# Kernel optimization log

Hardware: AMD Instinct MI355X
Metric: run time of the kernel (lower is better)

Reference implementation:

```python
import jax, jax.numpy as jnp
import numpy as np

N = 100000
E = 800000

def elu(x):
    return jnp.where(x > 0, x, jnp.expm1(x))

def transformer_conv(x, src, dst, ea, Wq, bq, Wk, bk, Wv, bv, We, Ws, bs, heads, ch):
    # PyG TransformerConv (concat=True, root_weight=True, beta=False, eval so dropout off)
    n = x.shape[0]
    q = (x @ Wq + bq).reshape(n, heads, ch)
    k = (x @ Wk + bk).reshape(n, heads, ch)
    v = (x @ Wv + bv).reshape(n, heads, ch)
    e = (ea @ We).reshape(-1, heads, ch)            # [E,H,C], lin_edge has no bias
    kj = k[src] + e                                  # [E,H,C]
    logits = (q[dst] * kj).sum(-1) / jnp.sqrt(jnp.float32(ch))  # [E,H]
    # segment softmax over incoming edges of each dst node
    m = jax.ops.segment_max(logits, dst, num_segments=n)
    ex = jnp.exp(logits - m[dst])
    denom = jax.ops.segment_sum(ex, dst, num_segments=n)
    alpha = ex / denom[dst]                          # [E,H]
    msg = alpha[..., None] * (v[src] + e)            # [E,H,C]
    agg = jax.ops.segment_sum(msg, dst, num_segments=n).reshape(n, heads * ch)
    return agg + x @ Ws + bs                         # skip connection (lin_skip)

def setup_inputs() -> dict:
    key = jax.random.key(0)
    ks = jax.random.split(key, 32)
    def rn(k, shape, scale=0.1):
        return jax.random.normal(k, shape, dtype=jnp.float32) * scale
    d = {}
    d['x'] = jax.random.normal(ks[0], (N, 23), dtype=jnp.float32)
    d['edge_index'] = jax.random.randint(ks[1], (2, E), 0, N, dtype=jnp.int32)
    d['edge_attr'] = jax.random.normal(ks[2], (E, 7), dtype=jnp.float32)
    d['linA_w'] = rn(ks[3], (23, 23)); d['linA_b'] = jnp.zeros((23,), jnp.float32)
    d['linB_w'] = rn(ks[4], (23, 23)); d['linB_b'] = jnp.zeros((23,), jnp.float32)
    # conv1: in=23, heads=8, out=24 -> 192
    d['q1_w'] = rn(ks[5], (23, 192)); d['q1_b'] = jnp.zeros((192,), jnp.float32)
    d['k1_w'] = rn(ks[6], (23, 192)); d['k1_b'] = jnp.zeros((192,), jnp.float32)
    d['v1_w'] = rn(ks[7], (23, 192)); d['v1_b'] = jnp.zeros((192,), jnp.float32)
    d['e1_w'] = rn(ks[8], (7, 192))
    d['s1_w'] = rn(ks[9], (23, 192)); d['s1_b'] = jnp.zeros((192,), jnp.float32)
    # conv4: in=192, heads=8, out=8 -> 64
    d['q2_w'] = rn(ks[10], (192, 64)); d['q2_b'] = jnp.zeros((64,), jnp.float32)
    d['k2_w'] = rn(ks[11], (192, 64)); d['k2_b'] = jnp.zeros((64,), jnp.float32)
    d['v2_w'] = rn(ks[12], (192, 64)); d['v2_b'] = jnp.zeros((64,), jnp.float32)
    d['e2_w'] = rn(ks[13], (7, 64))
    d['s2_w'] = rn(ks[14], (192, 64)); d['s2_b'] = jnp.zeros((64,), jnp.float32)
    d['lin1_w'] = rn(ks[15], (64, 20)); d['lin1_b'] = jnp.zeros((20,), jnp.float32)
    d['lin2_w'] = rn(ks[16], (20, 1)); d['lin2_b'] = jnp.zeros((1,), jnp.float32)
    return d

def reference(x, edge_index, edge_attr,
              linA_w, linA_b, linB_w, linB_b,
              q1_w, q1_b, k1_w, k1_b, v1_w, v1_b, e1_w, s1_w, s1_b,
              q2_w, q2_b, k2_w, k2_b, v2_w, v2_b, e2_w, s2_w, s2_b,
              lin1_w, lin1_b, lin2_w, lin2_b):
    src, dst = edge_index[0], edge_index[1]
    h = elu(x @ linA_w + linA_b)
    h = elu(h @ linB_w + linB_b)
    h = transformer_conv(h, src, dst, edge_attr, q1_w, q1_b, k1_w, k1_b, v1_w, v1_b, e1_w, s1_w, s1_b, 8, 24)
    h = elu(h)
    h = transformer_conv(h, src, dst, edge_attr, q2_w, q2_b, k2_w, k2_b, v2_w, v2_b, e2_w, s2_w, s2_b, 8, 8)
    h = elu(h)
    h = elu(h @ lin1_w + lin1_b)
    return h @ lin2_w + lin2_b
```

## Files before the change

kernel.cpp:

```cpp
#include <hip/hip_runtime.h>
#include <math.h>


__device__ __forceinline__ float elu_f(float x) {
    return x > 0.f ? x : expm1f(x);
}


__global__ void mlp_kernel(const float* __restrict__ x,
                           const float* __restrict__ A, const float* __restrict__ ab,
                           const float* __restrict__ B, const float* __restrict__ bb,
                           float* __restrict__ out, int n) {
    __shared__ float sA[23 * 23], sB[23 * 23], sa[23], sb[23];
    for (int t = threadIdx.x; t < 23 * 23; t += blockDim.x) { sA[t] = A[t]; sB[t] = B[t]; }
    if (threadIdx.x < 23) { sa[threadIdx.x] = ab[threadIdx.x]; sb[threadIdx.x] = bb[threadIdx.x]; }
    __syncthreads();
    int i = blockIdx.x * blockDim.x + threadIdx.x;
    if (i >= n) return;
    float xi[23], h1[23];
    #pragma unroll
    for (int j = 0; j < 23; j++) xi[j] = x[(size_t)i * 23 + j];
    #pragma unroll
    for (int o = 0; o < 23; o++) {
        float acc = sa[o];
        #pragma unroll
        for (int j = 0; j < 23; j++) acc = fmaf(xi[j], sA[j * 23 + o], acc);
        h1[o] = elu_f(acc);
    }
    #pragma unroll
    for (int o = 0; o < 23; o++) {
        float acc = sb[o];
        #pragma unroll
        for (int j = 0; j < 23; j++) acc = fmaf(h1[j], sB[j * 23 + o], acc);
        out[(size_t)i * 23 + o] = elu_f(acc);
    }
}

template<int IN, int Kc, int OUTW, int M, int TY, int KM, int VM>
__global__ void proj_tiled_kernel(const float* __restrict__ in, int n,
    const float* __restrict__ W0, const float* __restrict__ b0,
    const float* __restrict__ W1, const float* __restrict__ b1,
    const float* __restrict__ W2, const float* __restrict__ b2,
    const float* __restrict__ W3, const float* __restrict__ b3,
    float* __restrict__ kvout,
    float* __restrict__ r0, float* __restrict__ r1,
    float* __restrict__ r2, float* __restrict__ r3) {
    constexpr int WTOT = M * OUTW;
    constexpr int CG   = WTOT / 8;
    constexpr int BN   = TY * 4;
    constexpr int SAW  = BN + 4;
    constexpr int NT   = CG * TY;
    constexpr int PT   = OUTW / 4;
    static_assert(IN % Kc == 0, "Kc divides IN");
    __shared__ float sA[Kc][SAW];
    __shared__ float sB[Kc][WTOT];

    const int tid = threadIdx.x;
    const int tx = tid % CG;
    const int ty = tid / CG;
    const int node0 = blockIdx.x * BN;

    int colA, colB; bool pairkv; int chan0 = 0;
    if (tx < PT) {
        pairkv = true; chan0 = 4 * tx;
        colA = KM * OUTW + chan0;
        colB = VM * OUTW + chan0;
    } else {
        pairkv = false;
        int u = 8 * (tx - PT);
        auto remap = [&](int uu) {
            int ri = uu / OUTW, cc = uu - ri * OUTW;
            int cnt = 0, mat = 0;
            for (int mm = 0; mm < M; mm++) {
                if (mm == KM || mm == VM) continue;
                if (cnt == ri) { mat = mm; break; }
                cnt++;
            }
            return mat * OUTW + cc;
        };
        colA = remap(u); colB = remap(u + 4);
    }
    const int matA = colA / OUTW, ccA = colA % OUTW;
    const int matB = colB / OUTW, ccB = colB % OUTW;
    const float* bA = (matA == 0 ? b0 : matA == 1 ? b1 : matA == 2 ? b2 : b3);
    const float* bB = (matB == 0 ? b0 : matB == 1 ? b1 : matB == 2 ? b2 : b3);

    float acc[4][8];
    #pragma unroll
    for (int i = 0; i < 4; i++) {
        #pragma unroll
        for (int c = 0; c < 4; c++) { acc[i][c] = bA[ccA + c]; acc[i][4 + c] = bB[ccB + c]; }
    }

    for (int k0 = 0; k0 < IN; k0 += Kc) {
        for (int t = tid; t < Kc * BN; t += NT) {
            int j = t / BN, nn = t - j * BN;
            int g = node0 + nn;
            sA[j][nn] = (g < n) ? in[(size_t)g * IN + k0 + j] : 0.f;
        }
        for (int t = tid; t < Kc * WTOT; t += NT) {
            int j = t / WTOT, c = t - j * WTOT;
            int m = c / OUTW, cm = c - m * OUTW;
            const float* Wp = (m == 0 ? W0 : m == 1 ? W1 : m == 2 ? W2 : W3);
            sB[j][c] = Wp[(size_t)(k0 + j) * OUTW + cm];
        }
        __syncthreads();
        #pragma unroll 8
        for (int j = 0; j < Kc; j++) {
            float4 a  = *(const float4*)&sA[j][ty * 4];
            float4 v0 = *(const float4*)&sB[j][colA];
            float4 v1 = *(const float4*)&sB[j][colB];
            float av[4] = {a.x, a.y, a.z, a.w};
            float bv[8] = {v0.x, v0.y, v0.z, v0.w, v1.x, v1.y, v1.z, v1.w};
            #pragma unroll
            for (int i = 0; i < 4; i++)
                #pragma unroll
                for (int c = 0; c < 8; c++)
                    acc[i][c] = fmaf(av[i], bv[c], acc[i][c]);
        }
        __syncthreads();
    }

    #pragma unroll
    for (int i = 0; i < 4; i++) {
        int g = node0 + ty * 4 + i;
        if (g >= n) continue;
        if (pairkv) {
            float* kp = kvout + (size_t)g * (2 * OUTW) + 2 * chan0;
            *(float4*)(kp + 0) = make_float4(acc[i][0], acc[i][4], acc[i][1], acc[i][5]);
            *(float4*)(kp + 4) = make_float4(acc[i][2], acc[i][6], acc[i][3], acc[i][7]);
        } else {
            float* rA = (matA == 0 ? r0 : matA == 1 ? r1 : matA == 2 ? r2 : r3);
            float* rB = (matB == 0 ? r0 : matB == 1 ? r1 : matB == 2 ? r2 : r3);
            *(float4*)(rA + (size_t)g * OUTW + ccA) = make_float4(acc[i][0], acc[i][1], acc[i][2], acc[i][3]);
            *(float4*)(rB + (size_t)g * OUTW + ccB) = make_float4(acc[i][4], acc[i][5], acc[i][6], acc[i][7]);
        }
    }
}


__global__ void zero2_kernel(int* __restrict__ a, int* __restrict__ b, int n) {
    int i = blockIdx.x * blockDim.x + threadIdx.x;
    if (i < n) { a[i] = 0; b[i] = 0; }
}

__global__ void count_kernel(const int* __restrict__ dst, int* __restrict__ cnt, int nE) {
    int e = blockIdx.x * blockDim.x + threadIdx.x;
    if (e < nE) atomicAdd(&cnt[dst[e]], 1);
}

__global__ void scan_block_kernel(int* __restrict__ cnt, int* __restrict__ bsum, int n) {
    __shared__ int sdat[256];
    int i = blockIdx.x * 256 + threadIdx.x;
    int v = (i < n) ? cnt[i] : 0;
    sdat[threadIdx.x] = v;
    __syncthreads();
    for (int off = 1; off < 256; off <<= 1) {
        int t = (threadIdx.x >= (unsigned)off) ? sdat[threadIdx.x - off] : 0;
        __syncthreads();
        sdat[threadIdx.x] += t;
        __syncthreads();
    }
    if (i < n) cnt[i] = sdat[threadIdx.x] - v;
    if (threadIdx.x == 255) bsum[blockIdx.x] = sdat[255];
}

__global__ void scan_bsum_kernel(int* __restrict__ bsum, int nb) {
    __shared__ int s[1024];
    int i = threadIdx.x;
    int v = (i < nb) ? bsum[i] : 0;
    s[i] = v;
    __syncthreads();
    for (int off = 1; off < 1024; off <<= 1) {
        int t = (i >= off) ? s[i - off] : 0;
        __syncthreads();
        s[i] += t;
        __syncthreads();
    }
    if (i < nb) bsum[i] = s[i] - v;
}

__global__ void finalize_rp_kernel(const int* __restrict__ cnt, const int* __restrict__ bsum,
                                   int* __restrict__ rp, int n, int nE) {
    int i = blockIdx.x * blockDim.x + threadIdx.x;
    if (i < n) rp[i] = cnt[i] + bsum[i >> 8];
    if (i == n) rp[n] = nE;
}

__global__ void scatter_kernel(const int* __restrict__ src, const int* __restrict__ dst,
                               const int* __restrict__ rp, int* __restrict__ cur,
                               int* __restrict__ srcS, int* __restrict__ eidS, int nE) {
    int e = blockIdx.x * blockDim.x + threadIdx.x;
    if (e >= nE) return;
    int d = dst[e];
    int pos = rp[d] + atomicAdd(&cur[d], 1);
    srcS[pos] = src[e];
    eidS[pos] = e;
}

template<int IN, int C, bool QMAT, bool DOELU>
__global__ void conv_fused_kernel(const float* __restrict__ feat,
                                  const float* __restrict__ Wq, const float* __restrict__ qb,
                                  const float* __restrict__ kv,
                                  const float* __restrict__ qmat,
                                  const float* __restrict__ ea, const float* __restrict__ We,
                                  const int* __restrict__ rp, const int* __restrict__ srcS,
                                  const int* __restrict__ eidS,
                                  float* __restrict__ out, int n, float scale) {
    constexpr int HC = 8 * C;
    constexpr int CPL = HC / 64;
    constexpr int KVROW = 2 * HC;
    const int lane = threadIdx.x & 63;
    const int d = blockIdx.x * (blockDim.x >> 6) + (threadIdx.x >> 6);
    if (d >= n) return;
    const int ch0 = lane * CPL;

    float we[7][CPL];
    #pragma unroll
    for (int j = 0; j < 7; j++)
        #pragma unroll
        for (int c = 0; c < CPL; c++) we[j][c] = We[j * HC + ch0 + c];

    float* op = out + (size_t)d * HC + ch0;
    float sk[CPL], q[CPL];
    #pragma unroll
    for (int c = 0; c < CPL; c++) sk[c] = op[c];
    if constexpr (QMAT) {
        const float* qp = qmat + (size_t)d * HC + ch0;
        #pragma unroll
        for (int c = 0; c < CPL; c++) q[c] = qp[c];
    } else {
        #pragma unroll
        for (int c = 0; c < CPL; c++) q[c] = qb[ch0 + c];
        const float* fd = feat + (size_t)d * IN;
        for (int j = 0; j < IN; j++) {
            float f = fd[j];
            #pragma unroll
            for (int c = 0; c < CPL; c++)
                q[c] = fmaf(f, Wq[(size_t)j * HC + ch0 + c], q[c]);
        }
    }

    float m = -INFINITY, l = 0.f, acc[CPL];
    #pragma unroll
    for (int c = 0; c < CPL; c++) acc[c] = 0.f;

    const int p0 = rp[d], p1 = rp[d + 1];
    if (p0 < p1) {
        auto loadEdge = [&](int p, float* kc, float* vc, float* ev) {
            int s = srcS[p], eid = eidS[p];
            const float* pb = kv + (size_t)s * KVROW + 2 * ch0;
            #pragma unroll
            for (int c = 0; c < CPL; c++) {
                float2 t = *(const float2*)(pb + 2 * c);
                kc[c] = t.x; vc[c] = t.y;
            }
            const float* ep = ea + (size_t)eid * 7;
            #pragma unroll
            for (int j = 0; j < 7; j++) ev[j] = ep[j];
        };
        auto logitv = [&](const float* kc, const float* vc, const float* ev, float* vv) {
            float part = 0.f;
            #pragma unroll
            for (int c = 0; c < CPL; c++) {
                float ec = 0.f;
                #pragma unroll
                for (int j = 0; j < 7; j++) ec = fmaf(ev[j], we[j][c], ec);
                part = fmaf(q[c], kc[c] + ec, part);
                vv[c] = vc[c] + ec;
            }
            part += __shfl_xor(part, 1);
            part += __shfl_xor(part, 2);
            part += __shfl_xor(part, 4);
            return part * scale;
        };

        const int pL = p1 - 1;
        float k0a[CPL], v0a[CPL], e0a[7], k1a[CPL], v1a[CPL], e1a[7];
        loadEdge(p0, k0a, v0a, e0a);
        loadEdge((p0 + 1 < p1) ? p0 + 1 : pL, k1a, v1a, e1a);

        for (int p = p0; p < p1; p += 2) {
            float k2a[CPL], v2a[CPL], e2a[7], k3a[CPL], v3a[CPL], e3a[7];
            loadEdge((p + 2 < p1) ? p + 2 : pL, k2a, v2a, e2a);
            loadEdge((p + 3 < p1) ? p + 3 : pL, k3a, v3a, e3a);

            float vv0[CPL], vv1[CPL];
            float z0 = logitv(k0a, v0a, e0a, vv0);
            float z1 = logitv(k1a, v1a, e1a, vv1);
            if (p + 1 >= p1) z1 = -INFINITY;

            float mn = fmaxf(m, fmaxf(z0, z1));
            float rs  = expf(m - mn);
            float pw0 = expf(z0 - mn);
            float pw1 = expf(z1 - mn);
            l = fmaf(l, rs, pw0 + pw1);
            #pragma unroll
            for (int c = 0; c < CPL; c++)
                acc[c] = fmaf(acc[c], rs, fmaf(pw0, vv0[c], pw1 * vv1[c]));
            m = mn;

            #pragma unroll
            for (int c = 0; c < CPL; c++) {
                k0a[c] = k2a[c]; v0a[c] = v2a[c];
                k1a[c] = k3a[c]; v1a[c] = v3a[c];
            }
            #pragma unroll
            for (int j = 0; j < 7; j++) { e0a[j] = e2a[j]; e1a[j] = e3a[j]; }
        }
    }
    float invl = (l > 0.f) ? 1.f / l : 0.f;
    #pragma unroll
    for (int c = 0; c < CPL; c++) {
        float r = sk[c] + acc[c] * invl;
        op[c] = DOELU ? elu_f(r) : r;
    }
}

__global__ void head_kernel(const float* __restrict__ h, const float* __restrict__ W1,
                            const float* __restrict__ b1, const float* __restrict__ W2,
                            const float* __restrict__ b2, float* __restrict__ out, int n) {
    __shared__ float sW1[64 * 20], sb1[20], sW2[20], sb2;
    for (int t = threadIdx.x; t < 64 * 20; t += blockDim.x) sW1[t] = W1[t];
    if (threadIdx.x < 20) { sb1[threadIdx.x] = b1[threadIdx.x]; sW2[threadIdx.x] = W2[threadIdx.x]; }
    if (threadIdx.x == 0) sb2 = b2[0];
    __syncthreads();
    int i = blockIdx.x * blockDim.x + threadIdx.x;
    if (i >= n) return;
    float hv[64];
    const float* hp = h + (size_t)i * 64;
    #pragma unroll
    for (int j = 0; j < 64; j++) hv[j] = elu_f(hp[j]);
    float acc2 = sb2;
    for (int o = 0; o < 20; o++) {
        float a = sb1[o];
        #pragma unroll
        for (int j = 0; j < 64; j++) a = fmaf(hv[j], sW1[j * 20 + o], a);
        acc2 = fmaf(elu_f(a), sW2[o], acc2);
    }
    out[i] = acc2;
}

__global__ void zero_out_kernel(float* __restrict__ out, int n) {
    int i = blockIdx.x * blockDim.x + threadIdx.x;
    if (i < n) out[i] = 0.f;
}


extern "C" void kernel_launch(void* const* d_in, const int* in_sizes, int n_in,
                              void* d_out, int out_size, void* d_ws, size_t ws_size,
                              hipStream_t stream) {
    const float* x   = (const float*)d_in[0];
    const int*   ei  = (const int*)d_in[1];
    const float* ea  = (const float*)d_in[2];
    const float* Aw  = (const float*)d_in[3];
    const float* Ab  = (const float*)d_in[4];
    const float* Bw  = (const float*)d_in[5];
    const float* Bb  = (const float*)d_in[6];
    const float* q1w = (const float*)d_in[7];  const float* q1b = (const float*)d_in[8];
    const float* k1w = (const float*)d_in[9];  const float* k1b = (const float*)d_in[10];
    const float* v1w = (const float*)d_in[11]; const float* v1b = (const float*)d_in[12];
    const float* e1w = (const float*)d_in[13];
    const float* s1w = (const float*)d_in[14]; const float* s1b = (const float*)d_in[15];
    const float* q2w = (const float*)d_in[16]; const float* q2b = (const float*)d_in[17];
    const float* k2w = (const float*)d_in[18]; const float* k2b = (const float*)d_in[19];
    const float* v2w = (const float*)d_in[20]; const float* v2b = (const float*)d_in[21];
    const float* e2w = (const float*)d_in[22];
    const float* s2w = (const float*)d_in[23]; const float* s2b = (const float*)d_in[24];
    const float* l1w = (const float*)d_in[25]; const float* l1b = (const float*)d_in[26];
    const float* l2w = (const float*)d_in[27]; const float* l2b = (const float*)d_in[28];

    const int n  = in_sizes[0] / 23;
    const int nE = in_sizes[1] / 2;
    const int* src = ei;
    const int* dst = ei + nE;
    float* out = (float*)d_out;
    const int B = 256;
    const int nb = (n + 255) / 256;

    size_t fl_h1 = ((size_t)n * 23 + 3) & ~(size_t)3;
    size_t fl_o1 = (size_t)n * 192;
    size_t fl_kv = (size_t)n * 384;
    size_t ints_total = ((size_t)n + 1) + n + n + 1024 + (size_t)nE + (size_t)nE;
    size_t need_bytes = (fl_h1 + fl_o1 + fl_kv) * 4 + ints_total * 4;

    if (ws_size < need_bytes || nb > 1024) {
        zero_out_kernel<<<(out_size + B - 1) / B, B, 0, stream>>>(out, out_size);
        return;
    }

    float* ws = (float*)d_ws;
    size_t off = 0;
    float* h1    = ws + off; off += fl_h1;
    float* o1    = ws + off; off += fl_o1;
    float* kvreg = ws + off; off += fl_kv;
    int* ip = (int*)(ws + off);
    int* rp   = ip; ip += (size_t)n + 1;
    int* cnt  = ip; ip += n;
    int* cur  = ip; ip += n;
    int* bsum = ip; ip += 1024;
    int* srcS = ip; ip += nE;
    int* eidS = ip; ip += nE;

    float* kv1   = kvreg;
    float* kv2   = kvreg;
    float* q2buf = kvreg + (size_t)n * 128;
    float* o2    = kvreg + (size_t)n * 192;

    const float sc1 = 1.0f / sqrtf(24.0f);
    const float sc2 = 1.0f / sqrtf(8.0f);
    const float* np = nullptr;
    float* npw = nullptr;

    zero2_kernel<<<(n + B - 1) / B, B, 0, stream>>>(cnt, cur, n);
    count_kernel<<<(nE + B - 1) / B, B, 0, stream>>>(dst, cnt, nE);
    scan_block_kernel<<<nb, 256, 0, stream>>>(cnt, bsum, n);
    scan_bsum_kernel<<<1, 1024, 0, stream>>>(bsum, nb);
    finalize_rp_kernel<<<(n + 1 + B - 1) / B, B, 0, stream>>>(cnt, bsum, rp, n, nE);
    scatter_kernel<<<(nE + B - 1) / B, B, 0, stream>>>(src, dst, rp, cur, srcS, eidS, nE);

    mlp_kernel<<<(n + B - 1) / B, B, 0, stream>>>(x, Aw, Ab, Bw, Bb, h1, n);

    proj_tiled_kernel<23, 23, 192, 3, 8, 0, 1><<<(n + 31) / 32, 576, 0, stream>>>(
        h1, n, k1w, k1b, v1w, v1b, s1w, s1b, np, np,
        kv1, npw, npw, o1, npw);
    conv_fused_kernel<23, 24, false, true><<<(n + 3) / 4, 256, 0, stream>>>(
        h1, q1w, q1b, kv1, np, ea, e1w, rp, srcS, eidS, o1, n, sc1);

    proj_tiled_kernel<192, 32, 64, 4, 16, 1, 2><<<(n + 63) / 64, 512, 0, stream>>>(
        o1, n, q2w, q2b, k2w, k2b, v2w, v2b, s2w, s2b,
        kv2, q2buf, npw, npw, o2);
    conv_fused_kernel<192, 8, true, false><<<(n + 3) / 4, 256, 0, stream>>>(
        o1, q2w, q2b, kv2, q2buf, ea, e2w, rp, srcS, eidS, o2, n, sc2);

    head_kernel<<<(n + B - 1) / B, B, 0, stream>>>(o2, l1w, l1b, l2w, l2b, out, n);
}
```

Measured before the change: 1.302 ms.

## Rewrite projection GEMM with 8-node-by-CPT-column register tiles and interleaved KV columns

Replaces the projection kernel with a new tiling in which each thread accumulates 8 nodes by 12 or 8 output columns. Tiles cover 64 nodes, and block sizes change to 384 and 256 threads. K and V weight columns are interleaved directly in shared memory, so each thread's columns map to contiguous output and can be stored with float4 writes without the earlier pairing logic. The goal is higher arithmetic intensity per shared-memory load. In exchange it needs more accumulator registers, which may reduce occupancy.

New measurement: 1.423 ms. 9.3% more time.

```diff
diff --git a/kernel.cpp b/kernel.cpp
--- a/kernel.cpp
+++ b/kernel.cpp
@@ -36,60 +36,49 @@
     }
 }
 
-template<int IN, int Kc, int OUTW, int M, int TY, int KM, int VM>
-__global__ void proj_tiled_kernel(const float* __restrict__ in, int n,
-    const float* __restrict__ W0, const float* __restrict__ b0,
-    const float* __restrict__ W1, const float* __restrict__ b1,
-    const float* __restrict__ W2, const float* __restrict__ b2,
-    const float* __restrict__ W3, const float* __restrict__ b3,
-    float* __restrict__ kvout,
-    float* __restrict__ r0, float* __restrict__ r1,
-    float* __restrict__ r2, float* __restrict__ r3) {
-    constexpr int WTOT = M * OUTW;
-    constexpr int CG   = WTOT / 8;
-    constexpr int BN   = TY * 4;
+template<int CONFIG>
+__global__ void proj_gemm_kernel(const float* __restrict__ in, int n,
+    const float* __restrict__ Wq, const float* __restrict__ qb,
+    const float* __restrict__ Wk, const float* __restrict__ kb,
+    const float* __restrict__ Wv, const float* __restrict__ vb,
+    const float* __restrict__ Ws, const float* __restrict__ sb,
+    float* __restrict__ qout, float* __restrict__ kvout, float* __restrict__ sout) {
+    constexpr int IN   = (CONFIG == 1) ? 23 : 192;
+    constexpr int Kc   = (CONFIG == 1) ? 23 : 32;
+    constexpr int OUTW = (CONFIG == 1) ? 192 : 64;
+    constexpr int WTOT = (CONFIG == 1) ? 576 : 256;
+    constexpr int NT   = (CONFIG == 1) ? 384 : 256;
+    constexpr int CPT  = (CONFIG == 1) ? 12 : 8;
+    constexpr int BN   = 64;
     constexpr int SAW  = BN + 4;
-    constexpr int NT   = CG * TY;
-    constexpr int PT   = OUTW / 4;
-    static_assert(IN % Kc == 0, "Kc divides IN");
     __shared__ float sA[Kc][SAW];
     __shared__ float sB[Kc][WTOT];
 
     const int tid = threadIdx.x;
-    const int tx = tid % CG;
-    const int ty = tid / CG;
+    const int ng = tid & 7;
+    const int cg = tid >> 3;
     const int node0 = blockIdx.x * BN;
-
-    int colA, colB; bool pairkv; int chan0 = 0;
-    if (tx < PT) {
-        pairkv = true; chan0 = 4 * tx;
-        colA = KM * OUTW + chan0;
-        colB = VM * OUTW + chan0;
-    } else {
-        pairkv = false;
-        int u = 8 * (tx - PT);
-        auto remap = [&](int uu) {
-            int ri = uu / OUTW, cc = uu - ri * OUTW;
-            int cnt = 0, mat = 0;
-            for (int mm = 0; mm < M; mm++) {
-                if (mm == KM || mm == VM) continue;
-                if (cnt == ri) { mat = mm; break; }
-                cnt++;
-            }
-            return mat * OUTW + cc;
-        };
-        colA = remap(u); colB = remap(u + 4);
-    }
-    const int matA = colA / OUTW, ccA = colA % OUTW;
-    const int matB = colB / OUTW, ccB = colB % OUTW;
-    const float* bA = (matA == 0 ? b0 : matA == 1 ? b1 : matA == 2 ? b2 : b3);
-    const float* bB = (matB == 0 ? b0 : matB == 1 ? b1 : matB == 2 ? b2 : b3);
-
-    float acc[4][8];
-    #pragma unroll
-    for (int i = 0; i < 4; i++) {
-        #pragma unroll
-        for (int c = 0; c < 4; c++) { acc[i][c] = bA[ccA + c]; acc[i][4 + c] = bB[ccB + c]; }
+    const int c0 = CPT * cg;
+
+    auto wmap = [&](int c, const float*& W, const float*& b, int& wc) {
+        if constexpr (CONFIG == 1) {
+            if (c < 384) { W = (c & 1) ? Wv : Wk; b = (c & 1) ? vb : kb; wc = c >> 1; }
+            else         { W = Ws; b = sb; wc = c - 384; }
+        } else {
+            if (c < 64)       { W = Wq; b = qb; wc = c; }
+            else if (c < 192) { int u = c - 64; W = (u & 1) ? Wv : Wk; b = (u & 1) ? vb : kb; wc = u >> 1; }
+            else              { W = Ws; b = sb; wc = c - 192; }
+        }
+    };
+
+    float acc[8][CPT];
+    #pragma unroll
+    for (int ci = 0; ci < CPT; ci++) {
+        const float *W, *b; int wc;
+        wmap(c0 + ci, W, b, wc);
+        float bv = b[wc];
+        #pragma unroll
+        for (int ni = 0; ni < 8; ni++) acc[ni][ci] = bv;
     }
 
     for (int k0 = 0; k0 < IN; k0 += Kc) {
@@ -100,41 +89,49 @@
         }
         for (int t = tid; t < Kc * WTOT; t += NT) {
             int j = t / WTOT, c = t - j * WTOT;
-            int m = c / OUTW, cm = c - m * OUTW;
-            const float* Wp = (m == 0 ? W0 : m == 1 ? W1 : m == 2 ? W2 : W3);
-            sB[j][c] = Wp[(size_t)(k0 + j) * OUTW + cm];
-        }
-        __syncthreads();
-        #pragma unroll 8
+            const float *W, *b; int wc;
+            wmap(c, W, b, wc);
+            sB[j][c] = W[(size_t)(k0 + j) * OUTW + wc];
+        }
+        __syncthreads();
+        #pragma unroll 4
         for (int j = 0; j < Kc; j++) {
-            float4 a  = *(const float4*)&sA[j][ty * 4];
-            float4 v0 = *(const float4*)&sB[j][colA];
-            float4 v1 = *(const float4*)&sB[j][colB];
-            float av[4] = {a.x, a.y, a.z, a.w};
-            float bv[8] = {v0.x, v0.y, v0.z, v0.w, v1.x, v1.y, v1.z, v1.w};
-            #pragma unroll
-            for (int i = 0; i < 4; i++)
+            float4 a0 = *(const float4*)&sA[j][8 * ng];
+            float4 a1 = *(const float4*)&sA[j][8 * ng + 4];
+            float av[8] = {a0.x, a0.y, a0.z, a0.w, a1.x, a1.y, a1.z, a1.w};
+            float bv[CPT];
+            #pragma unroll
+            for (int i = 0; i < CPT / 4; i++) {
+                float4 t4 = *(const float4*)&sB[j][c0 + 4 * i];
+                bv[4 * i] = t4.x; bv[4 * i + 1] = t4.y; bv[4 * i + 2] = t4.z; bv[4 * i + 3] = t4.w;
+            }
+            #pragma unroll
+            for (int ni = 0; ni < 8; ni++)
                 #pragma unroll
-                for (int c = 0; c < 8; c++)
-                    acc[i][c] = fmaf(av[i], bv[c], acc[i][c]);
-        }
-        __syncthreads();
-    }
-
-    #pragma unroll
-    for (int i = 0; i < 4; i++) {
-        int g = node0 + ty * 4 + i;
+                for (int ci = 0; ci < CPT; ci++)
+                    acc[ni][ci] = fmaf(av[ni], bv[ci], acc[ni][ci]);
+        }
+        __syncthreads();
+    }
+
+    float* obase; int ostride, ocoff;
+    if constexpr (CONFIG == 1) {
+        if (c0 < 384) { obase = kvout; ostride = 384; ocoff = c0; }
+        else          { obase = sout;  ostride = 192; ocoff = c0 - 384; }
+    } else {
+        if (c0 < 64)       { obase = qout;  ostride = 64;  ocoff = c0; }
+        else if (c0 < 192) { obase = kvout; ostride = 128; ocoff = c0 - 64; }
+        else               { obase = sout;  ostride = 64;  ocoff = c0 - 192; }
+    }
+    #pragma unroll
+    for (int ni = 0; ni < 8; ni++) {
+        int g = node0 + 8 * ng + ni;
         if (g >= n) continue;
-        if (pairkv) {
-            float* kp = kvout + (size_t)g * (2 * OUTW) + 2 * chan0;
-            *(float4*)(kp + 0) = make_float4(acc[i][0], acc[i][4], acc[i][1], acc[i][5]);
-            *(float4*)(kp + 4) = make_float4(acc[i][2], acc[i][6], acc[i][3], acc[i][7]);
-        } else {
-            float* rA = (matA == 0 ? r0 : matA == 1 ? r1 : matA == 2 ? r2 : r3);
-            float* rB = (matB == 0 ? r0 : matB == 1 ? r1 : matB == 2 ? r2 : r3);
-            *(float4*)(rA + (size_t)g * OUTW + ccA) = make_float4(acc[i][0], acc[i][1], acc[i][2], acc[i][3]);
-            *(float4*)(rB + (size_t)g * OUTW + ccB) = make_float4(acc[i][4], acc[i][5], acc[i][6], acc[i][7]);
-        }
+        float* op = obase + (size_t)g * ostride + ocoff;
+        #pragma unroll
+        for (int i = 0; i < CPT / 4; i++)
+            *(float4*)(op + 4 * i) = make_float4(acc[ni][4 * i], acc[ni][4 * i + 1],
+                                                 acc[ni][4 * i + 2], acc[ni][4 * i + 3]);
     }
 }
 
@@ -421,15 +418,17 @@
 
     mlp_kernel<<<(n + B - 1) / B, B, 0, stream>>>(x, Aw, Ab, Bw, Bb, h1, n);
 
-    proj_tiled_kernel<23, 23, 192, 3, 8, 0, 1><<<(n + 31) / 32, 576, 0, stream>>>(
-        h1, n, k1w, k1b, v1w, v1b, s1w, s1b, np, np,
-        kv1, npw, npw, o1, npw);
+    const int gproj = (n + 63) / 64;
+
+    proj_gemm_kernel<1><<<gproj, 384, 0, stream>>>(
+        h1, n, np, np, k1w, k1b, v1w, v1b, s1w, s1b,
+        npw, kv1, o1);
     conv_fused_kernel<23, 24, false, true><<<(n + 3) / 4, 256, 0, stream>>>(
         h1, q1w, q1b, kv1, np, ea, e1w, rp, srcS, eidS, o1, n, sc1);
 
-    proj_tiled_kernel<192, 32, 64, 4, 16, 1, 2><<<(n + 63) / 64, 512, 0, stream>>>(
+    proj_gemm_kernel<2><<<gproj, 256, 0, stream>>>(
         o1, n, q2w, q2b, k2w, k2b, v2w, v2b, s2w, s2b,
-        kv2, q2buf, npw, npw, o2);
+        q2buf, kv2, o2);
     conv_fused_kernel<192, 8, true, false><<<(n + 3) / 4, 256, 0, stream>>>(
         o1, q2w, q2b, kv2, q2buf, ea, e2w, rp, srcS, eidS, o2, n, sc2);
 
```
